# Optimization experiments

Measured on AMD Instinct MI355X. Metric: run time of the kernel, lower is better.

The kernel has to match this reference:

```python
import jax, jax.numpy as jnp
import numpy as np
from jax import lax

MODES = 16
DEPTH = 8
NPH = 8  # photons = sum(init_state); init_state = [1]*8 + [0]*8
IDX = np.arange(NPH)  # output_indices derived from init_state
PI = np.pi
CHUNK = 4096  # pairs per permanent chunk (memory control, mirrors chunk_subsets idea)


def setup_inputs() -> dict:
    key = jax.random.key(0)
    k1, k2, k3 = jax.random.split(key, 3)
    x = jax.random.normal(k1, (256, 64), dtype=jnp.float32)
    W = jax.random.normal(k2, (120, 64), dtype=jnp.float32) / np.sqrt(64.0)
    b = jax.random.normal(k3, (120,), dtype=jnp.float32) * 0.01
    return {"x": x, "W": W, "b": b}


def _forward(x, W, b):
    N = x.shape[0]
    # fc1 + sigmoid embedding -> angle pairs
    x_emb = jax.nn.sigmoid(x @ W.T + b)              # (N, 120)
    tbu = x_emb.reshape(N, -1, 2)                    # (N, T, 2)
    theta = tbu[:, :, 0] * (PI / 2)
    phi = tbu[:, :, 1] * (2 * PI)
    ct = jnp.cos(theta).astype(jnp.complex64)
    st = jnp.sin(theta).astype(jnp.complex64)
    ep = jnp.exp(1j * phi.astype(jnp.complex64))
    # 2x2 tunable beam-splitter unitaries: [[e^{i phi} c, -s], [e^{i phi} s, c]]
    row0 = jnp.stack([ep * ct, -st], axis=-1)
    row1 = jnp.stack([ep * st, ct], axis=-1)
    blocks = jnp.stack([row0, row1], axis=-2)        # (N, T, 2, 2)

    # Apply block-diagonal layers. Block-diag matmul only mixes row pairs,
    # so update row segments directly instead of building (modes,modes) UBS.
    U = jnp.broadcast_to(jnp.eye(MODES, dtype=jnp.complex64), (N, MODES, MODES))
    nb_even, nb_odd = MODES // 2, (MODES - 2) // 2
    n_before = 0
    for d in range(DEPTH):
        if d % 2 == 0:
            nb, off = nb_even, 0
        else:
            nb, off = nb_odd, 1
        blk = blocks[:, n_before:n_before + nb]                      # (N, nb, 2, 2)
        seg = U[:, off:off + 2 * nb, :].reshape(N, nb, 2, MODES)     # row pairs
        new = jnp.einsum('nkab,nkbm->nkam', blk, seg).reshape(N, 2 * nb, MODES)
        U = U.at[:, off:off + 2 * nb, :].set(new)
        n_before += nb

    # Photonic Gram: K[a,b] = |perm( (U_a^dag U_b)[idx, idx] )|^2.
    # Only the idx-columns of U enter: V = U[:, :, idx], submatrix = V_a^dag V_b.
    V = U[:, :, IDX]                                  # (N, MODES, n)
    G = jnp.einsum('ami,bmj->abij', V.conj(), V)      # (N, N, n, n)

    n = NPH
    subsets = jnp.arange(1, 1 << n)                   # (S,), S = 2^n - 1
    masks = (subsets[:, None] >> jnp.arange(n)[None, :]) & 1   # (S, n)
    signs = (1 - 2 * ((n - masks.sum(axis=1)) & 1)).astype(jnp.complex64)
    maskc = masks.astype(jnp.complex64)

    A = G.reshape(N * N, n, n)
    nc = (N * N) // CHUNK

    def perm_chunk(Ac):  # Ryser: sum_S (-1)^{n-|S|} prod_i sum_{j in S} A_ij
        ss = jnp.einsum('cij,sj->csi', Ac, maskc)     # (c, S, n) subset row-sums
        pr = jnp.prod(ss, axis=2)                     # (c, S)
        return jnp.sum(pr * signs, axis=1)            # (c,)

    perms = lax.map(perm_chunk, A.reshape(nc, CHUNK, n, n)).reshape(N * N)
    K = (jnp.abs(perms) ** 2).astype(jnp.float32).reshape(N, N)
    di = jnp.arange(N)
    K = K.at[di, di].set(1.0)
    return x_emb, K


def reference(x, W, b):
    return _forward(x, W, b)
```

## Files before the change

### kernel.cpp

```cpp
#include <hip/hip_runtime.h>
#include <math.h>

#define NS 256
#define EMB 120
#define NBLK 60
#define MODES 16
#define NPH 8

__device__ __forceinline__ float2 cmul(float2 a, float2 b) {
    float2 r;
    r.x = fmaf(a.x, b.x, -(a.y * b.y));
    r.y = fmaf(a.x, b.y,   a.y * b.x);
    return r;
}

__global__ __launch_bounds__(128) void emb_v_kernel(
    const float* __restrict__ x, const float* __restrict__ W,
    const float* __restrict__ bias, float* __restrict__ out_emb,
    float2* __restrict__ Vws)
{
    const int s = blockIdx.x;
    const int t = threadIdx.x;
    __shared__ float emb[EMB];
    __shared__ float ctA[NBLK], stA[NBLK], exA[NBLK], eyA[NBLK];

    if (t < EMB) {
        const float* xr = x + s * 64;
        const float* wr = W + t * 64;
        float acc = bias[t];
        #pragma unroll
        for (int k = 0; k < 64; ++k) acc = fmaf(xr[k], wr[k], acc);
        float e = 1.0f / (1.0f + expf(-acc));
        emb[t] = e;
        out_emb[s * EMB + t] = e;
    }
    __syncthreads();

    if (t < NBLK) {
        float th = emb[2 * t]     * 1.57079632679489662f;
        float ph = emb[2 * t + 1] * 6.28318530717958648f;
        float st, ct, sp, cp;
        sincosf(th, &st, &ct);
        sincosf(ph, &sp, &cp);
        ctA[t] = ct; stA[t] = st; exA[t] = cp; eyA[t] = sp;
    }
    __syncthreads();

    if (t < NPH) {
        const int c = t;
        float2 u[MODES];
        #pragma unroll
        for (int m = 0; m < MODES; ++m) {
            u[m].x = (m == c) ? 1.0f : 0.0f;
            u[m].y = 0.0f;
        }
        int bi = 0;
        #pragma unroll
        for (int d = 0; d < 8; ++d) {
            const int off = d & 1;
            const int nb = 8 - off;
            #pragma unroll
            for (int k = 0; k < nb; ++k) {
                float ct = ctA[bi], st = stA[bi], ex = exA[bi], ey = eyA[bi];
                ++bi;
                const int r0 = off + 2 * k;
                float2 u0 = u[r0], u1 = u[r0 + 1];
                float2 n0, n1;
                n0.x = ex * ct * u0.x - ey * ct * u0.y - st * u1.x;
                n0.y = ex * ct * u0.y + ey * ct * u0.x - st * u1.y;
                n1.x = ex * st * u0.x - ey * st * u0.y + ct * u1.x;
                n1.y = ex * st * u0.y + ey * st * u0.x + ct * u1.y;
                u[r0] = n0; u[r0 + 1] = n1;
            }
        }
        #pragma unroll
        for (int m = 0; m < MODES; ++m)
            Vws[(s * MODES + m) * NPH + c] = u[m];
    }
}

__global__ __launch_bounds__(256) void perm_kernel(
    const float2* __restrict__ Vws, float* __restrict__ outK)
{
    __shared__ float2 lds_a[16][130];
    __shared__ float2 lds_b[16][130];

    const int tid = threadIdx.x;
    const int ta = blockIdx.x >> 4;
    const int tb = blockIdx.x & 15;

    const float4* srcA = (const float4*)(Vws + (size_t)ta * 16 * 128);
    const float4* srcB = (const float4*)(Vws + (size_t)tb * 16 * 128);
    #pragma unroll
    for (int q = 0; q < 4; ++q) {
        int idx = q * 256 + tid;
        int row = idx >> 6;
        int pos = (idx & 63) * 2;
        float4 fa = srcA[idx];
        float4 fb = srcB[idx];
        lds_a[row][pos].x     = fa.x; lds_a[row][pos].y     = fa.y;
        lds_a[row][pos + 1].x = fa.z; lds_a[row][pos + 1].y = fa.w;
        lds_b[row][pos].x     = fb.x; lds_b[row][pos].y     = fb.y;
        lds_b[row][pos + 1].x = fb.z; lds_b[row][pos + 1].y = fb.w;
    }
    __syncthreads();

    const int tx = tid & 15;
    const int ty = tid >> 4;

    float2 G[8][8];
    #pragma unroll
    for (int i = 0; i < 8; ++i)
        #pragma unroll
        for (int j = 0; j < 8; ++j) { G[i][j].x = 0.f; G[i][j].y = 0.f; }

    #pragma unroll 1
    for (int m = 0; m < 16; ++m) {
        float2 va[8], vb[8];
        #pragma unroll
        for (int i = 0; i < 8; ++i) va[i] = lds_a[ty][m * 8 + i];
        #pragma unroll
        for (int j = 0; j < 8; ++j) vb[j] = lds_b[tx][m * 8 + j];
        #pragma unroll
        for (int i = 0; i < 8; ++i)
            #pragma unroll
            for (int j = 0; j < 8; ++j) {
                G[i][j].x = fmaf(va[i].x, vb[j].x, fmaf(va[i].y, vb[j].y, G[i][j].x));
                G[i][j].y = fmaf(va[i].x, vb[j].y, fmaf(-va[i].y, vb[j].x, G[i][j].y));
            }
    }

    float2 rs[8];
    #pragma unroll
    for (int i = 0; i < 8; ++i) { rs[i].x = 0.f; rs[i].y = 0.f; }
    float2 acc; acc.x = 0.f; acc.y = 0.f;

#define RSTEP(J, S, TS) do {                                          \
        _Pragma("unroll")                                             \
        for (int i = 0; i < 8; ++i) {                                 \
            rs[i].x = fmaf((S), G[i][J].x, rs[i].x);                  \
            rs[i].y = fmaf((S), G[i][J].y, rs[i].y);                  \
        }                                                             \
        float2 p01 = cmul(rs[0], rs[1]);                              \
        float2 p23 = cmul(rs[2], rs[3]);                              \
        float2 p45 = cmul(rs[4], rs[5]);                              \
        float2 p67 = cmul(rs[6], rs[7]);                              \
        float2 q0  = cmul(p01, p23);                                  \
        float2 q1  = cmul(p45, p67);                                  \
        float2 pr  = cmul(q0, q1);                                    \
        acc.x = fmaf((TS), pr.x, acc.x);                              \
        acc.y = fmaf((TS), pr.y, acc.y);                              \
    } while (0)

    #pragma unroll 1
    for (int o = 0; o < 16; ++o) {
        const float s8 = (o & 1) ? -1.f : 1.f;
        RSTEP(0,  1.f, -1.f);
        RSTEP(1,  1.f,  1.f);
        RSTEP(0, -1.f, -1.f);
        RSTEP(2,  1.f,  1.f);
        RSTEP(0,  1.f, -1.f);
        RSTEP(1, -1.f,  1.f);
        RSTEP(0, -1.f, -1.f);
        RSTEP(3,  s8,   1.f);
        RSTEP(0,  1.f, -1.f);
        RSTEP(1,  1.f,  1.f);
        RSTEP(0, -1.f, -1.f);
        RSTEP(2, -1.f,  1.f);
        RSTEP(0,  1.f, -1.f);
        RSTEP(1, -1.f,  1.f);
        RSTEP(0, -1.f, -1.f);
        if (o < 15) {
            const int p = o + 1;
            const int jj = __builtin_ctz(p);
            const float s16 = ((p >> (jj + 1)) & 1) ? -1.f : 1.f;
            float2 col[8];
            #pragma unroll
            for (int i = 0; i < 8; ++i) {
                float2 s01 = (jj & 1) ? G[i][5] : G[i][4];
                float2 s23 = (jj & 1) ? G[i][7] : G[i][6];
                col[i] = (jj & 2) ? s23 : s01;
            }
            #pragma unroll
            for (int i = 0; i < 8; ++i) {
                rs[i].x = fmaf(s16, col[i].x, rs[i].x);
                rs[i].y = fmaf(s16, col[i].y, rs[i].y);
            }
            float2 p01 = cmul(rs[0], rs[1]);
            float2 p23 = cmul(rs[2], rs[3]);
            float2 p45 = cmul(rs[4], rs[5]);
            float2 p67 = cmul(rs[6], rs[7]);
            float2 q0  = cmul(p01, p23);
            float2 q1  = cmul(p45, p67);
            float2 pr  = cmul(q0, q1);
            acc.x += pr.x;
            acc.y += pr.y;
        }
    }
#undef RSTEP

    const int a = ta * 16 + ty;
    const int b = tb * 16 + tx;
    float K = fmaf(acc.x, acc.x, acc.y * acc.y);
    if (a == b) K = 1.0f;
    outK[a * 256 + b] = K;
}

extern "C" void kernel_launch(void* const* d_in, const int* in_sizes, int n_in,
                              void* d_out, int out_size, void* d_ws, size_t ws_size,
                              hipStream_t stream) {
    const float* x    = (const float*)d_in[0];
    const float* W    = (const float*)d_in[1];
    const float* bias = (const float*)d_in[2];
    float* out     = (float*)d_out;
    float* out_emb = out;
    float* outK    = out + NS * EMB;
    float2* Vws    = (float2*)d_ws;

    emb_v_kernel<<<NS, 128, 0, stream>>>(x, W, bias, out_emb, Vws);
    perm_kernel<<<NS, 256, 0, stream>>>(Vws, outK);
}
```

Before: 89.50 us.

## Replace Ryser subset sum with Glynn formula Gray-code permanent

Computes the 8x8 permanent with Glynn's formula, using ±1 sign vectors in Gray-code order, instead of Ryser's subset enumeration. This halves the number of product-tree evaluations, from 255 to 128. Row sums start as full sums and are updated by ±2 times a column, and the final |perm|^2 is rescaled by 1/2^14. Launch bounds also request a minimum of one block per CU, which lets the compiler use more registers. Float rounding changes slightly because of the different summation order.

```diff
diff --git a/kernel.cpp b/kernel.cpp
--- a/kernel.cpp
+++ b/kernel.cpp
@@ -79,7 +79,7 @@
     }
 }
 
-__global__ __launch_bounds__(256) void perm_kernel(
+__global__ __launch_bounds__(256, 1) void perm_kernel(
     const float2* __restrict__ Vws, float* __restrict__ outK)
 {
     __shared__ float2 lds_a[16][130];
@@ -132,76 +132,71 @@
 
     float2 rs[8];
     #pragma unroll
-    for (int i = 0; i < 8; ++i) { rs[i].x = 0.f; rs[i].y = 0.f; }
-    float2 acc; acc.x = 0.f; acc.y = 0.f;
-
-#define RSTEP(J, S, TS) do {                                          \
-        _Pragma("unroll")                                             \
-        for (int i = 0; i < 8; ++i) {                                 \
-            rs[i].x = fmaf((S), G[i][J].x, rs[i].x);                  \
-            rs[i].y = fmaf((S), G[i][J].y, rs[i].y);                  \
-        }                                                             \
+    for (int i = 0; i < 8; ++i) {
+        float sx = 0.f, sy = 0.f;
+        #pragma unroll
+        for (int j = 0; j < 8; ++j) { sx += G[i][j].x; sy += G[i][j].y; }
+        rs[i].x = sx; rs[i].y = sy;
+    }
+
+    float2 acc;
+
+#define PRODTREE(OUT) do {                                            \
         float2 p01 = cmul(rs[0], rs[1]);                              \
         float2 p23 = cmul(rs[2], rs[3]);                              \
         float2 p45 = cmul(rs[4], rs[5]);                              \
         float2 p67 = cmul(rs[6], rs[7]);                              \
         float2 q0  = cmul(p01, p23);                                  \
         float2 q1  = cmul(p45, p67);                                  \
-        float2 pr  = cmul(q0, q1);                                    \
+        OUT = cmul(q0, q1);                                           \
+    } while (0)
+
+#define UPD(J, S) do {                                                \
+        _Pragma("unroll")                                             \
+        for (int i = 0; i < 8; ++i) {                                 \
+            rs[i].x = fmaf((S), G[i][J].x, rs[i].x);                  \
+            rs[i].y = fmaf((S), G[i][J].y, rs[i].y);                  \
+        }                                                             \
+    } while (0)
+
+#define TERM(TS) do {                                                 \
+        float2 pr; PRODTREE(pr);                                      \
         acc.x = fmaf((TS), pr.x, acc.x);                              \
         acc.y = fmaf((TS), pr.y, acc.y);                              \
     } while (0)
 
+    PRODTREE(acc);
+
     #pragma unroll 1
-    for (int o = 0; o < 16; ++o) {
-        const float s8 = (o & 1) ? -1.f : 1.f;
-        RSTEP(0,  1.f, -1.f);
-        RSTEP(1,  1.f,  1.f);
-        RSTEP(0, -1.f, -1.f);
-        RSTEP(2,  1.f,  1.f);
-        RSTEP(0,  1.f, -1.f);
-        RSTEP(1, -1.f,  1.f);
-        RSTEP(0, -1.f, -1.f);
-        RSTEP(3,  s8,   1.f);
-        RSTEP(0,  1.f, -1.f);
-        RSTEP(1,  1.f,  1.f);
-        RSTEP(0, -1.f, -1.f);
-        RSTEP(2, -1.f,  1.f);
-        RSTEP(0,  1.f, -1.f);
-        RSTEP(1, -1.f,  1.f);
-        RSTEP(0, -1.f, -1.f);
-        if (o < 15) {
-            const int p = o + 1;
-            const int jj = __builtin_ctz(p);
-            const float s16 = ((p >> (jj + 1)) & 1) ? -1.f : 1.f;
-            float2 col[8];
-            #pragma unroll
-            for (int i = 0; i < 8; ++i) {
-                float2 s01 = (jj & 1) ? G[i][5] : G[i][4];
-                float2 s23 = (jj & 1) ? G[i][7] : G[i][6];
-                col[i] = (jj & 2) ? s23 : s01;
+    for (int p = 0; p < 16; ++p) {
+        const float s4 = (p & 1) ? 2.f : -2.f;
+        UPD(1, -2.f); TERM(-1.f);
+        UPD(2, -2.f); TERM( 1.f);
+        UPD(1,  2.f); TERM(-1.f);
+        UPD(3,  s4 ); TERM( 1.f);
+        UPD(1, -2.f); TERM(-1.f);
+        UPD(2,  2.f); TERM( 1.f);
+        UPD(1,  2.f); TERM(-1.f);
+        if (p < 15) {
+            const int q = p + 1;
+            const int c = __builtin_ctz(q);
+            const float s = ((q >> (c + 1)) & 1) ? 2.f : -2.f;
+            switch (c) {
+                case 0: UPD(4, s); break;
+                case 1: UPD(5, s); break;
+                case 2: UPD(6, s); break;
+                default: UPD(7, s); break;
             }
-            #pragma unroll
-            for (int i = 0; i < 8; ++i) {
-                rs[i].x = fmaf(s16, col[i].x, rs[i].x);
-                rs[i].y = fmaf(s16, col[i].y, rs[i].y);
-            }
-            float2 p01 = cmul(rs[0], rs[1]);
-            float2 p23 = cmul(rs[2], rs[3]);
-            float2 p45 = cmul(rs[4], rs[5]);
-            float2 p67 = cmul(rs[6], rs[7]);
-            float2 q0  = cmul(p01, p23);
-            float2 q1  = cmul(p45, p67);
-            float2 pr  = cmul(q0, q1);
-            acc.x += pr.x;
-            acc.y += pr.y;
+            TERM(1.f);
         }
     }
-#undef RSTEP
+#undef UPD
+#undef TERM
+#undef PRODTREE
 
     const int a = ta * 16 + ty;
     const int b = tb * 16 + tx;
-    float K = fmaf(acc.x, acc.x, acc.y * acc.y);
+    float K = fmaf(acc.x, acc.x, acc.y * acc.y) * (1.0f / 16384.0f);
     if (a == b) K = 1.0f;
     outK[a * 256 + b] = K;
 }
```

Result: faster. 80.89 us (-9.6%).
